# Kernel tuning notes

Hardware: AMD Instinct MI355X
Metric: run time of the kernel (lower is better)

## Reference

```python
import jax, jax.numpy as jnp
import numpy as np

N = 20000
E = 320000
IN_DIM, HID, OUT_DIM = 32, 64, 4
HEADS = 4
NEG_SLOPE = 0.2


def _self_loops(src, dst):
    loop = jnp.arange(N, dtype=src.dtype)
    return jnp.concatenate([src, loop]), jnp.concatenate([dst, loop])


def gcn_conv(x, W, b, src, dst):
    h = x @ W                                            # [N, C]
    es, ed = _self_loops(src, dst)
    deg = jax.ops.segment_sum(jnp.ones_like(es, dtype=h.dtype), ed, num_segments=N)
    dinv = jnp.where(deg > 0, jax.lax.rsqrt(deg), 0.0)
    norm = dinv[es] * dinv[ed]                           # [E']
    out = jax.ops.segment_sum(h[es] * norm[:, None], ed, num_segments=N)
    return out + b


def gat_conv(x, W, att_src, att_dst, b, src, dst):
    # PyG GATConv: heads concat, self-loops, leaky_relu(0.2), softmax over incoming edges per dst
    H, C = att_src.shape
    h = (x @ W).reshape(N, H, C)                         # [N, H, C]
    a_s = jnp.sum(h * att_src, axis=-1)                  # [N, H]
    a_d = jnp.sum(h * att_dst, axis=-1)                  # [N, H]
    es, ed = _self_loops(src, dst)
    logits = jax.nn.leaky_relu(a_s[es] + a_d[ed], NEG_SLOPE)   # [E', H]
    m = jax.ops.segment_max(logits, ed, num_segments=N)
    expv = jnp.exp(logits - m[ed])
    denom = jax.ops.segment_sum(expv, ed, num_segments=N)
    alpha = expv / denom[ed]                             # [E', H]
    out = jax.ops.segment_sum(h[es] * alpha[:, :, None], ed, num_segments=N)
    return out.reshape(N, H * C) + b


def setup_inputs() -> dict:
    key = jax.random.key(0)
    ks = iter(jax.random.split(key, 32))
    s = 0.05
    def w(shape):
        return jax.random.normal(next(ks), shape, dtype=jnp.float32) * s
    inp = {}
    inp["x"] = jax.random.normal(next(ks), (N, IN_DIM), dtype=jnp.float32)
    inp["edge_index"] = jax.random.randint(next(ks), (2, E), 0, N, dtype=jnp.int32)
    # encoder1 GCN 32->64; encoder2 GCN 64->128; encoder3 GAT 128->128 x4 heads
    inp["w_e1"], inp["b_e1"] = w((IN_DIM, HID)), jnp.zeros((HID,), jnp.float32)
    inp["w_e2"], inp["b_e2"] = w((HID, 2 * HID)), jnp.zeros((2 * HID,), jnp.float32)
    inp["w_e3"] = w((2 * HID, HEADS * 2 * HID))
    inp["as_e3"], inp["ad_e3"] = w((HEADS, 2 * HID)), w((HEADS, 2 * HID))
    inp["b_e3"] = jnp.zeros((HEADS * 2 * HID,), jnp.float32)
    # decoder1 GCN 1024->128; decoder2 GCN 128->64; decoder3 GAT 64->64 x4 heads
    inp["w_d1"], inp["b_d1"] = w((HEADS * 2 * HID, 2 * HID)), jnp.zeros((2 * HID,), jnp.float32)
    inp["w_d2"], inp["b_d2"] = w((2 * HID, HID)), jnp.zeros((HID,), jnp.float32)
    inp["w_d3"] = w((HID, HEADS * HID))
    inp["as_d3"], inp["ad_d3"] = w((HEADS, HID)), w((HEADS, HID))
    inp["b_d3"] = jnp.zeros((HEADS * HID,), jnp.float32)
    # MLP head 256->256->128->4
    inp["w_fc1"], inp["b_fc1"] = w((4 * HID, 4 * HID)), jnp.zeros((4 * HID,), jnp.float32)
    inp["w_fc2"], inp["b_fc2"] = w((4 * HID, 2 * HID)), jnp.zeros((2 * HID,), jnp.float32)
    inp["w_fin"], inp["b_fin"] = w((2 * HID, OUT_DIM)), jnp.zeros((OUT_DIM,), jnp.float32)
    return inp


def reference(x, edge_index, w_e1, b_e1, w_e2, b_e2, w_e3, as_e3, ad_e3, b_e3,
              w_d1, b_d1, w_d2, b_d2, w_d3, as_d3, ad_d3, b_d3,
              w_fc1, b_fc1, w_fc2, b_fc2, w_fin, b_fin):
    src, dst = edge_index[0], edge_index[1]
    relu = jax.nn.relu
    x1 = relu(gcn_conv(x, w_e1, b_e1, src, dst))
    x2 = relu(gcn_conv(x1, w_e2, b_e2, src, dst))
    x3 = relu(gat_conv(x2, w_e3, as_e3, ad_e3, b_e3, src, dst))
    h = relu(gcn_conv(x3, w_d1, b_d1, src, dst)) + x2
    h = relu(gcn_conv(h, w_d2, b_d2, src, dst)) + x1
    h = relu(gat_conv(h, w_d3, as_d3, ad_d3, b_d3, src, dst))
    h = relu(h @ w_fc1 + b_fc1)
    h = relu(h @ w_fc2 + b_fc2)
    return h @ w_fin + b_fin
```

## Files before the change

### kernel.cpp

```cpp
#include <hip/hip_runtime.h>
#include <cstdint>
#include <cstddef>

static constexpr int Nn = 20000;
static constexpr int Ee = 320000;

typedef _Float16 half8 __attribute__((ext_vector_type(8)));
typedef float f32x4 __attribute__((ext_vector_type(4)));

__device__ __forceinline__ float lrelu02(float x){ return fmaxf(x, 0.2f*x); }
__device__ __forceinline__ float af(int x){ return __int_as_float(x); }

__device__ __forceinline__ void packhl(float v, unsigned short& h, unsigned short& l){
  _Float16 hh = (_Float16)v;
  _Float16 ll = (_Float16)((v - (float)hh) * 2048.0f);
  h = __builtin_bit_cast(unsigned short, hh);
  l = __builtin_bit_cast(unsigned short, ll);
}

__global__ void k_count(const int* __restrict__ dst, int* __restrict__ cnt){
  int e = blockIdx.x*256 + threadIdx.x;
  if (e < Ee) atomicAdd(&cnt[dst[e]], 1);
}

__global__ void k_scan(const int* __restrict__ cnt, int* __restrict__ row_start,
                       float* __restrict__ dinv){
  __shared__ int part[1024];
  int tid = threadIdx.x;
  const int PER = 20;
  int base = tid*PER;
  int s = 0;
  for (int i = 0; i < PER; ++i){ int idx = base+i; if (idx < Nn) s += cnt[idx]; }
  part[tid] = s; __syncthreads();
  for (int off = 1; off < 1024; off <<= 1){
    int v = (tid >= off) ? part[tid-off] : 0;
    __syncthreads();
    part[tid] += v;
    __syncthreads();
  }
  int run = (tid == 0) ? 0 : part[tid-1];
  for (int i = 0; i < PER; ++i){
    int idx = base+i;
    if (idx < Nn){
      row_start[idx] = run;
      int c = cnt[idx];
      run += c;
      dinv[idx] = rsqrtf((float)(c+1));
    }
  }
  if (tid == 1023) row_start[Nn] = run;
}

__global__ void k_scatter(const int* __restrict__ src, const int* __restrict__ dst,
                          const int* __restrict__ row_start, int* __restrict__ fill,
                          int* __restrict__ csr){
  int e = blockIdx.x*256 + threadIdx.x;
  if (e < Ee){
    int d = dst[e];
    int pos = row_start[d] + atomicAdd(&fill[d], 1);
    csr[pos] = src[e];
  }
}

__global__ void k_erec(const int* __restrict__ csr, const float* __restrict__ dinv,
                       int2* __restrict__ erec){
  int i = blockIdx.x*256 + threadIdx.x;
  if (i < Ee){
    int u = csr[i];
    erec[i] = make_int2(u, __float_as_int(dinv[u]));
  }
}

template<int K, int J>
__global__ void k_packwf(const float* __restrict__ W, unsigned short* __restrict__ out){
  int i = blockIdx.x*256 + threadIdx.x;
  if (i < K*J){
    int k = i / J, col = i - k*J;
    unsigned short h, l; packhl(W[i], h, l);
    size_t pos = ((size_t)((col>>4)*(K/8) + (k>>3))*16 + (col&15))*8 + (k&7);
    out[pos] = h;
    out[pos + (size_t)K*J] = l;
  }
}

template<int C, int POST>
__global__ __launch_bounds__(256) void k_gcn_agg(
    const float* __restrict__ h, const float* __restrict__ dinv,
    const int* __restrict__ row_start, const int2* __restrict__ erec,
    const float* __restrict__ bias, const float* __restrict__ skip,
    float* __restrict__ outf, unsigned short* __restrict__ outp){
  int v = blockIdx.x*4 + (threadIdx.x >> 6);
  int lane = threadIdx.x & 63;
  int s = __builtin_amdgcn_readfirstlane(row_start[v]);
  int e = __builtin_amdgcn_readfirstlane(row_start[v+1]);
  float dv = dinv[v];
  const int c = (C==32) ? (lane & 31) : ((C==128) ? lane*2 : lane);

  float a0 = 0.f, a1 = 0.f;
  if constexpr (C == 32){
    int half = lane >> 5;
    int j = s + half;
    for (; j + 2 < e; j += 4){
      int2 r0 = erec[j], r1 = erec[j+2];
      float t0 = h[(size_t)r0.x*32 + c];
      float t1 = h[(size_t)r1.x*32 + c];
      a0 = fmaf(af(r0.y), t0, a0);
      a0 = fmaf(af(r1.y), t1, a0);
    }
    if (j < e){
      int2 r0 = erec[j];
      a0 = fmaf(af(r0.y), h[(size_t)r0.x*32 + c], a0);
    }
    a0 += __shfl_xor(a0, 32);
  } else if constexpr (C == 128){
    int j = s;
    for (; j + 4 <= e; j += 4){
      int2 r0 = erec[j], r1 = erec[j+1], r2 = erec[j+2], r3 = erec[j+3];
      float2 t0 = *(const float2*)&h[(size_t)r0.x*128 + c];
      float2 t1 = *(const float2*)&h[(size_t)r1.x*128 + c];
      float2 t2 = *(const float2*)&h[(size_t)r2.x*128 + c];
      float2 t3 = *(const float2*)&h[(size_t)r3.x*128 + c];
      a0=fmaf(af(r0.y),t0.x,a0); a1=fmaf(af(r0.y),t0.y,a1);
      a0=fmaf(af(r1.y),t1.x,a0); a1=fmaf(af(r1.y),t1.y,a1);
      a0=fmaf(af(r2.y),t2.x,a0); a1=fmaf(af(r2.y),t2.y,a1);
      a0=fmaf(af(r3.y),t3.x,a0); a1=fmaf(af(r3.y),t3.y,a1);
    }
    for (; j < e; ++j){
      int2 r = erec[j];
      float2 t = *(const float2*)&h[(size_t)r.x*128 + c];
      a0 = fmaf(af(r.y), t.x, a0); a1 = fmaf(af(r.y), t.y, a1);
    }
  } else {
    int j = s;
    for (; j + 4 <= e; j += 4){
      int2 r0 = erec[j], r1 = erec[j+1], r2 = erec[j+2], r3 = erec[j+3];
      float t0 = h[(size_t)r0.x*64 + c];
      float t1 = h[(size_t)r1.x*64 + c];
      float t2 = h[(size_t)r2.x*64 + c];
      float t3 = h[(size_t)r3.x*64 + c];
      a0=fmaf(af(r0.y),t0,a0); a0=fmaf(af(r1.y),t1,a0);
      a0=fmaf(af(r2.y),t2,a0); a0=fmaf(af(r3.y),t3,a0);
    }
    for (; j < e; ++j){
      int2 r = erec[j];
      a0 = fmaf(af(r.y), h[(size_t)r.x*64 + c], a0);
    }
  }

  if constexpr (C == 128){
    float2 hv = *(const float2*)&h[(size_t)v*128 + c];
    float vx = fmaf(a0, dv, hv.x*dv*dv);
    float vy = fmaf(a1, dv, hv.y*dv*dv);
    if constexpr (POST & 1){
      float2 bv = *(const float2*)&bias[c];
      float2 sk = *(const float2*)&skip[(size_t)v*128 + c];
      vx = fmaxf(vx + bv.x, 0.f) + sk.x;
      vy = fmaxf(vy + bv.y, 0.f) + sk.y;
    }
    if constexpr (POST & 2){
      unsigned short h0,l0,h1,l1; packhl(vx,h0,l0); packhl(vy,h1,l1);
      *(unsigned int*)&outp[(size_t)v*128 + c] = (unsigned)h0 | ((unsigned)h1<<16);
      *(unsigned int*)&outp[(size_t)v*128 + c + (size_t)Nn*128] = (unsigned)l0 | ((unsigned)l1<<16);
    } else {
      *(float2*)&outf[(size_t)v*128 + c] = make_float2(vx, vy);
    }
  } else if constexpr (C == 64){
    float val = fmaf(a0, dv, h[(size_t)v*64 + c]*dv*dv);
    if constexpr (POST & 1){
      val = fmaxf(val + bias[c], 0.f) + skip[(size_t)v*64 + c];
    }
    if constexpr (POST & 2){
      unsigned short hh,ll; packhl(val,hh,ll);
      outp[(size_t)v*64 + c] = hh;
      outp[(size_t)v*64 + c + (size_t)Nn*64] = ll;
    } else {
      outf[(size_t)v*64 + c] = val;
    }
  } else {
    float val = fmaf(a0, dv, h[(size_t)v*32 + c]*dv*dv);
    if (lane < 32){
      unsigned short hh,ll; packhl(val,hh,ll);
      outp[(size_t)v*32 + c] = hh;
      outp[(size_t)v*32 + c + (size_t)Nn*32] = ll;
    }
  }
}

template<int INC, int C>
__global__ void k_fold(const float* __restrict__ W, const float* __restrict__ as_,
                       const float* __restrict__ ad_, float* __restrict__ wsF,
                       float* __restrict__ wdF){
  int h = threadIdx.x >> 6, lane = threadIdx.x & 63;
  for (int k = lane; k < INC; k += 64){
    float s = 0.f, d = 0.f;
    #pragma unroll 4
    for (int c = 0; c < C; ++c){
      float wv = W[(size_t)k*(4*C) + h*C + c];
      s = fmaf(wv, as_[h*C + c], s);
      d = fmaf(wv, ad_[h*C + c], d);
    }
    wsF[h*INC + k] = s;
    wdF[h*INC + k] = d;
  }
}

template<int INC>
__global__ __launch_bounds__(256) void k_attn_in(
    const float* __restrict__ X, const float* __restrict__ wsF, const float* __restrict__ wdF,
    float* __restrict__ aS, float* __restrict__ aD){
  int v = blockIdx.x*4 + (threadIdx.x >> 6);
  int lane = threadIdx.x & 63;
  float x0 = X[(size_t)v*INC + lane];
  float x1 = (INC == 128) ? X[(size_t)v*INC + 64 + lane] : 0.f;
  float s[4], d[4];
  #pragma unroll
  for (int h = 0; h < 4; ++h){
    s[h] = x0*wsF[h*INC + lane];
    d[h] = x0*wdF[h*INC + lane];
    if constexpr (INC == 128){
      s[h] = fmaf(x1, wsF[h*INC + 64 + lane], s[h]);
      d[h] = fmaf(x1, wdF[h*INC + 64 + lane], d[h]);
    }
  }
  #pragma unroll
  for (int off = 32; off; off >>= 1){
    #pragma unroll
    for (int h = 0; h < 4; ++h){
      s[h] += __shfl_xor(s[h], off);
      d[h] += __shfl_xor(d[h], off);
    }
  }
  if (lane == 0){
    *(float4*)&aS[v*4] = make_float4(s[0], s[1], s[2], s[3]);
    *(float4*)&aD[v*4] = make_float4(d[0], d[1], d[2], d[3]);
  }
}

__global__ __launch_bounds__(256) void k_gat_prep(
    const float* __restrict__ aS, const float* __restrict__ aD,
    const int* __restrict__ row_start, const int* __restrict__ csr,
    float4* __restrict__ alphaE, float4* __restrict__ fS4, float4* __restrict__ rin4){
  int v = blockIdx.x*4 + (threadIdx.x >> 6);
  int lane = threadIdx.x & 63;
  int s = row_start[v], e = row_start[v+1];

  float4 tD = *(const float4*)&aD[v*4];
  float ad0=tD.x, ad1=tD.y, ad2=tD.z, ad3=tD.w;
  float4 tS = *(const float4*)&aS[v*4];
  float ls0=lrelu02(tS.x+ad0), ls1=lrelu02(tS.y+ad1), ls2=lrelu02(tS.z+ad2), ls3=lrelu02(tS.w+ad3);

  float m0=ls0, m1=ls1, m2=ls2, m3=ls3;
  for (int i = s + lane; i < e; i += 64){
    int u = csr[i];
    float4 a4 = *(const float4*)&aS[u*4];
    m0 = fmaxf(m0, lrelu02(a4.x+ad0));
    m1 = fmaxf(m1, lrelu02(a4.y+ad1));
    m2 = fmaxf(m2, lrelu02(a4.z+ad2));
    m3 = fmaxf(m3, lrelu02(a4.w+ad3));
  }
  #pragma unroll
  for (int off = 32; off; off >>= 1){
    m0 = fmaxf(m0, __shfl_xor(m0, off));
    m1 = fmaxf(m1, __shfl_xor(m1, off));
    m2 = fmaxf(m2, __shfl_xor(m2, off));
    m3 = fmaxf(m3, __shfl_xor(m3, off));
  }

  float sd0=0.f, sd1=0.f, sd2=0.f, sd3=0.f;
  for (int i = s + lane; i < e; i += 64){
    int u = csr[i];
    float4 a4 = *(const float4*)&aS[u*4];
    float f0 = __expf(lrelu02(a4.x+ad0) - m0);
    float f1 = __expf(lrelu02(a4.y+ad1) - m1);
    float f2 = __expf(lrelu02(a4.z+ad2) - m2);
    float f3 = __expf(lrelu02(a4.w+ad3) - m3);
    sd0 += f0; sd1 += f1; sd2 += f2; sd3 += f3;
    alphaE[i] = make_float4(f0, f1, f2, f3);
  }
  #pragma unroll
  for (int off = 32; off; off >>= 1){
    sd0 += __shfl_xor(sd0, off);
    sd1 += __shfl_xor(sd1, off);
    sd2 += __shfl_xor(sd2, off);
    sd3 += __shfl_xor(sd3, off);
  }
  if (lane == 0){
    float es0=__expf(ls0-m0), es1=__expf(ls1-m1), es2=__expf(ls2-m2), es3=__expf(ls3-m3);
    fS4[v] = make_float4(es0, es1, es2, es3);
    rin4[v] = make_float4(1.f/(sd0+es0), 1.f/(sd1+es1), 1.f/(sd2+es2), 1.f/(sd3+es3));
  }
}

template<int INC>
__global__ __launch_bounds__(256) void k_gat_agg2(
    const float* __restrict__ X, const int* __restrict__ csr,
    const float4* __restrict__ alphaE, const float4* __restrict__ fS4,
    const float4* __restrict__ rin4, const int* __restrict__ row_start,
    unsigned short* __restrict__ outp){
  int v = blockIdx.x*4 + (threadIdx.x >> 6);
  int lane = threadIdx.x & 63;
  int s = __builtin_amdgcn_readfirstlane(row_start[v]);
  int e = __builtin_amdgcn_readfirstlane(row_start[v+1]);
  const int c2 = lane*2;

  float2 acc0={0,0}, acc1={0,0}, acc2={0,0}, acc3={0,0};
  float ac0=0.f, ac1=0.f, ac2=0.f, ac3=0.f;

  int j = s;
  for (; j + 4 <= e; j += 4){
    int u0=csr[j], u1=csr[j+1], u2=csr[j+2], u3=csr[j+3];
    float4 f0=alphaE[j], f1=alphaE[j+1], f2=alphaE[j+2], f3=alphaE[j+3];
    if constexpr (INC == 128){
      float2 x0 = *(const float2*)&X[(size_t)u0*128 + c2];
      float2 x1 = *(const float2*)&X[(size_t)u1*128 + c2];
      float2 x2 = *(const float2*)&X[(size_t)u2*128 + c2];
      float2 x3 = *(const float2*)&X[(size_t)u3*128 + c2];
      acc0.x=fmaf(f0.x,x0.x,acc0.x); acc0.y=fmaf(f0.x,x0.y,acc0.y);
      acc1.x=fmaf(f0.y,x0.x,acc1.x); acc1.y=fmaf(f0.y,x0.y,acc1.y);
      acc2.x=fmaf(f0.z,x0.x,acc2.x); acc2.y=fmaf(f0.z,x0.y,acc2.y);
      acc3.x=fmaf(f0.w,x0.x,acc3.x); acc3.y=fmaf(f0.w,x0.y,acc3.y);
      acc0.x=fmaf(f1.x,x1.x,acc0.x); acc0.y=fmaf(f1.x,x1.y,acc0.y);
      acc1.x=fmaf(f1.y,x1.x,acc1.x); acc1.y=fmaf(f1.y,x1.y,acc1.y);
      acc2.x=fmaf(f1.z,x1.x,acc2.x); acc2.y=fmaf(f1.z,x1.y,acc2.y);
      acc3.x=fmaf(f1.w,x1.x,acc3.x); acc3.y=fmaf(f1.w,x1.y,acc3.y);
      acc0.x=fmaf(f2.x,x2.x,acc0.x); acc0.y=fmaf(f2.x,x2.y,acc0.y);
      acc1.x=fmaf(f2.y,x2.x,acc1.x); acc1.y=fmaf(f2.y,x2.y,acc1.y);
      acc2.x=fmaf(f2.z,x2.x,acc2.x); acc2.y=fmaf(f2.z,x2.y,acc2.y);
      acc3.x=fmaf(f2.w,x2.x,acc3.x); acc3.y=fmaf(f2.w,x2.y,acc3.y);
      acc0.x=fmaf(f3.x,x3.x,acc0.x); acc0.y=fmaf(f3.x,x3.y,acc0.y);
      acc1.x=fmaf(f3.y,x3.x,acc1.x); acc1.y=fmaf(f3.y,x3.y,acc1.y);
      acc2.x=fmaf(f3.z,x3.x,acc2.x); acc2.y=fmaf(f3.z,x3.y,acc2.y);
      acc3.x=fmaf(f3.w,x3.x,acc3.x); acc3.y=fmaf(f3.w,x3.y,acc3.y);
    } else {
      float x0 = X[(size_t)u0*64 + lane];
      float x1 = X[(size_t)u1*64 + lane];
      float x2 = X[(size_t)u2*64 + lane];
      float x3 = X[(size_t)u3*64 + lane];
      ac0=fmaf(f0.x,x0,ac0); ac1=fmaf(f0.y,x0,ac1); ac2=fmaf(f0.z,x0,ac2); ac3=fmaf(f0.w,x0,ac3);
      ac0=fmaf(f1.x,x1,ac0); ac1=fmaf(f1.y,x1,ac1); ac2=fmaf(f1.z,x1,ac2); ac3=fmaf(f1.w,x1,ac3);
      ac0=fmaf(f2.x,x2,ac0); ac1=fmaf(f2.y,x2,ac1); ac2=fmaf(f2.z,x2,ac2); ac3=fmaf(f2.w,x2,ac3);
      ac0=fmaf(f3.x,x3,ac0); ac1=fmaf(f3.y,x3,ac1); ac2=fmaf(f3.z,x3,ac2); ac3=fmaf(f3.w,x3,ac3);
    }
  }
  for (; j < e; ++j){
    int u = csr[j];
    float4 f = alphaE[j];
    if constexpr (INC == 128){
      float2 xu = *(const float2*)&X[(size_t)u*128 + c2];
      acc0.x=fmaf(f.x,xu.x,acc0.x); acc0.y=fmaf(f.x,xu.y,acc0.y);
      acc1.x=fmaf(f.y,xu.x,acc1.x); acc1.y=fmaf(f.y,xu.y,acc1.y);
      acc2.x=fmaf(f.z,xu.x,acc2.x); acc2.y=fmaf(f.z,xu.y,acc2.y);
      acc3.x=fmaf(f.w,xu.x,acc3.x); acc3.y=fmaf(f.w,xu.y,acc3.y);
    } else {
      float xu = X[(size_t)u*64 + lane];
      ac0=fmaf(f.x,xu,ac0); ac1=fmaf(f.y,xu,ac1); ac2=fmaf(f.z,xu,ac2); ac3=fmaf(f.w,xu,ac3);
    }
  }

  float4 fs = fS4[v];
  float4 rv = rin4[v];

  if constexpr (INC == 128){
    float2 xv = *(const float2*)&X[(size_t)v*128 + c2];
    const size_t loOff = (size_t)Nn*512;
    float ox, oy; unsigned short h0,l0,h1,l1;
    ox=(acc0.x+fs.x*xv.x)*rv.x; oy=(acc0.y+fs.x*xv.y)*rv.x;
    packhl(ox,h0,l0); packhl(oy,h1,l1);
    *(unsigned int*)&outp[(size_t)v*512 +   0 + c2] = (unsigned)h0|((unsigned)h1<<16);
    *(unsigned int*)&outp[(size_t)v*512 +   0 + c2 + loOff] = (unsigned)l0|((unsigned)l1<<16);
    ox=(acc1.x+fs.y*xv.x)*rv.y; oy=(acc1.y+fs.y*xv.y)*rv.y;
    packhl(ox,h0,l0); packhl(oy,h1,l1);
    *(unsigned int*)&outp[(size_t)v*512 + 128 + c2] = (unsigned)h0|((unsigned)h1<<16);
    *(unsigned int*)&outp[(size_t)v*512 + 128 + c2 + loOff] = (unsigned)l0|((unsigned)l1<<16);
    ox=(acc2.x+fs.z*xv.x)*rv.z; oy=(acc2.y+fs.z*xv.y)*rv.z;
    packhl(ox,h0,l0); packhl(oy,h1,l1);
    *(unsigned int*)&outp[(size_t)v*512 + 256 + c2] = (unsigned)h0|((unsigned)h1<<16);
    *(unsigned int*)&outp[(size_t)v*512 + 256 + c2 + loOff] = (unsigned)l0|((unsigned)l1<<16);
    ox=(acc3.x+fs.w*xv.x)*rv.w; oy=(acc3.y+fs.w*xv.y)*rv.w;
    packhl(ox,h0,l0); packhl(oy,h1,l1);
    *(unsigned int*)&outp[(size_t)v*512 + 384 + c2] = (unsigned)h0|((unsigned)h1<<16);
    *(unsigned int*)&outp[(size_t)v*512 + 384 + c2 + loOff] = (unsigned)l0|((unsigned)l1<<16);
  } else {
    float xv = X[(size_t)v*64 + lane];
    const size_t loOff = (size_t)Nn*256;
    unsigned short hh,ll;
    float o;
    o = (ac0+fs.x*xv)*rv.x; packhl(o,hh,ll);
    outp[(size_t)v*256 +   0 + lane] = hh; outp[(size_t)v*256 +   0 + lane + loOff] = ll;
    o = (ac1+fs.y*xv)*rv.y; packhl(o,hh,ll);
    outp[(size_t)v*256 +  64 + lane] = hh; outp[(size_t)v*256 +  64 + lane + loOff] = ll;
    o = (ac2+fs.z*xv)*rv.z; packhl(o,hh,ll);
    outp[(size_t)v*256 + 128 + lane] = hh; outp[(size_t)v*256 + 128 + lane + loOff] = ll;
    o = (ac3+fs.w*xv)*rv.w; packhl(o,hh,ll);
    outp[(size_t)v*256 + 192 + lane] = hh; outp[(size_t)v*256 + 192 + lane + loOff] = ll;
  }
}

template<int K, int J, int Jh, int EPI>
__global__ __launch_bounds__(256) void k_gemm(
    const unsigned short* __restrict__ Ahi, int lda,
    const unsigned short* __restrict__ Wp,
    const float* __restrict__ bias,
    float* __restrict__ outf, unsigned short* __restrict__ outp){
  __shared__ unsigned short sAhi[2*64*8], sAlo[2*64*8];
  __shared__ unsigned short sBhi[4*64*8], sBlo[4*64*8];

  const int tid  = threadIdx.x;
  const int lane = tid & 63, w = tid >> 6;
  const int rh = w & 1, ch = w >> 1;
  const int rb = blockIdx.x;
  const int colbase = blockIdx.z*Jh + blockIdx.y*64;
  const int akoff   = blockIdx.z*K;
  const size_t AloOff = (size_t)Nn*lda;
  const size_t WloOff = (size_t)K*J;

  f32x4 accH0 = {0,0,0,0}, accH1 = {0,0,0,0};
  f32x4 accM0 = {0,0,0,0}, accM1 = {0,0,0,0};

  const int arow = tid >> 3;
  const int ak4  = (tid & 7) * 4;
  const int aw_idx = (((arow>>4)*4 + (ak4>>3))*16 + (arow&15))*8 + (ak4&4);
  const unsigned short* Ag = Ahi + (size_t)(rb*32 + arow)*lda + akoff + ak4;
  const int bcol = tid & 63;
  const int bkg  = tid >> 6;
  const int bw_idx = (((bcol>>4)*4 + bkg)*16 + (bcol&15))*8;
  const int cf_g  = (colbase>>4) + (bcol>>4);
  const size_t wbase = ((size_t)cf_g*(K/8)*16 + (size_t)(bcol&15))*8;

  #pragma unroll 1
  for (int ks = 0; ks < K/32; ++ks){
    if (ks) __syncthreads();
    {
      const unsigned short* p = Ag + ks*32;
      uint2 hv = *(const uint2*)p;
      uint2 lv = *(const uint2*)(p + AloOff);
      *(uint2*)&sAhi[aw_idx] = hv;
      *(uint2*)&sAlo[aw_idx] = lv;
    }
    {
      size_t goff = wbase + (size_t)(ks*4 + bkg)*16*8;
      uint4 hv = *(const uint4*)&Wp[goff];
      uint4 lv = *(const uint4*)&Wp[goff + WloOff];
      *(uint4*)&sBhi[bw_idx] = hv;
      *(uint4*)&sBlo[bw_idx] = lv;
    }
    __syncthreads();

    half8 aH = *(const half8*)&sAhi[(rh*64 + lane)*8];
    half8 aL = *(const half8*)&sAlo[(rh*64 + lane)*8];
    {
      int cf = ch*2;
      half8 bH = *(const half8*)&sBhi[(cf*64 + lane)*8];
      half8 bL = *(const half8*)&sBlo[(cf*64 + lane)*8];
      accH0 = __builtin_amdgcn_mfma_f32_16x16x32_f16(aH, bH, accH0, 0, 0, 0);
      accM0 = __builtin_amdgcn_mfma_f32_16x16x32_f16(aH, bL, accM0, 0, 0, 0);
      accM0 = __builtin_amdgcn_mfma_f32_16x16x32_f16(aL, bH, accM0, 0, 0, 0);
    }
    {
      int cf = ch*2 + 1;
      half8 bH = *(const half8*)&sBhi[(cf*64 + lane)*8];
      half8 bL = *(const half8*)&sBlo[(cf*64 + lane)*8];
      accH1 = __builtin_amdgcn_mfma_f32_16x16x32_f16(aH, bH, accH1, 0, 0, 0);
      accM1 = __builtin_amdgcn_mfma_f32_16x16x32_f16(aH, bL, accM1, 0, 0, 0);
      accM1 = __builtin_amdgcn_mfma_f32_16x16x32_f16(aL, bH, accM1, 0, 0, 0);
    }
  }

  #pragma unroll
  for (int q = 0; q < 2; ++q){
    int cf = ch*2 + q;
    int col = colbase + cf*16 + (lane & 15);
    float bv = (EPI >= 1) ? bias[col] : 0.f;
    const f32x4& aH = q ? accH1 : accH0;
    const f32x4& aM = q ? accM1 : accM0;
    #pragma unroll
    for (int r = 0; r < 4; ++r){
      int row = rb*32 + rh*16 + ((lane>>4)*4 + r);
      float v = aH[r] + aM[r]*(1.0f/2048.0f);
      if constexpr (EPI >= 1) v = fmaxf(v + bv, 0.f);
      if constexpr (EPI == 2){
        unsigned short hh, ll; packhl(v, hh, ll);
        outp[(size_t)row*J + col] = hh;
        outp[(size_t)row*J + col + (size_t)Nn*J] = ll;
      } else {
        outf[(size_t)row*J + col] = v;
      }
    }
  }
}

__global__ __launch_bounds__(256) void k_mm_fin(
    const float* __restrict__ A, const float* __restrict__ W,
    const float* __restrict__ bias, float* __restrict__ out){
  int row = blockIdx.x*4 + (threadIdx.x >> 6);
  int lane = threadIdx.x & 63;
  float a0 = A[(size_t)row*128 + lane];
  float a1 = A[(size_t)row*128 + 64 + lane];
  float4 w0 = ((const float4*)W)[lane];
  float4 w1 = ((const float4*)W)[64 + lane];
  float p0 = fmaf(a1, w1.x, a0*w0.x);
  float p1 = fmaf(a1, w1.y, a0*w0.y);
  float p2 = fmaf(a1, w1.z, a0*w0.z);
  float p3 = fmaf(a1, w1.w, a0*w0.w);
  #pragma unroll
  for (int off = 32; off; off >>= 1){
    p0 += __shfl_xor(p0, off);
    p1 += __shfl_xor(p1, off);
    p2 += __shfl_xor(p2, off);
    p3 += __shfl_xor(p3, off);
  }
  if (lane == 0){
    float4 bv = *(const float4*)bias;
    *(float4*)&out[(size_t)row*4] = make_float4(p0+bv.x, p1+bv.y, p2+bv.z, p3+bv.w);
  }
}

extern "C" void kernel_launch(void* const* d_in, const int* in_sizes, int n_in,
                              void* d_out, int out_size, void* d_ws, size_t ws_size,
                              hipStream_t stream){
  const float* x     = (const float*)d_in[0];
  const int*   ei    = (const int*)  d_in[1];
  const float* w_e1  = (const float*)d_in[2];
  const float* b_e1  = (const float*)d_in[3];
  const float* w_e2  = (const float*)d_in[4];
  const float* b_e2  = (const float*)d_in[5];
  const float* w_e3  = (const float*)d_in[6];
  const float* as_e3 = (const float*)d_in[7];
  const float* ad_e3 = (const float*)d_in[8];
  const float* b_e3  = (const float*)d_in[9];
  const float* w_d1  = (const float*)d_in[10];
  const float* b_d1  = (const float*)d_in[11];
  const float* w_d2  = (const float*)d_in[12];
  const float* b_d2  = (const float*)d_in[13];
  const float* w_d3  = (const float*)d_in[14];
  const float* as_d3 = (const float*)d_in[15];
  const float* ad_d3 = (const float*)d_in[16];
  const float* b_d3  = (const float*)d_in[17];
  const float* w_fc1 = (const float*)d_in[18];
  const float* b_fc1 = (const float*)d_in[19];
  const float* w_fc2 = (const float*)d_in[20];
  const float* b_fc2 = (const float*)d_in[21];
  const float* w_fin = (const float*)d_in[22];
  const float* b_fin = (const float*)d_in[23];

  char* ws = (char*)d_ws;
  size_t off = 0;
  auto alloc = [&](size_t bytes)->char*{
    char* p = ws + off;
    off += (bytes + 127) & ~size_t(127);
    return p;
  };
  int*   cnt       = (int*)  alloc((size_t)Nn*4);
  int*   fill      = (int*)  alloc((size_t)Nn*4);
  int*   row_start = (int*)  alloc((size_t)(Nn+1)*4);
  int*   csr       = (int*)  alloc((size_t)Ee*4);
  float* dinv      = (float*)alloc((size_t)Nn*4);
  int2*  erec      = (int2*) alloc((size_t)Ee*8);
  float4* alphaE   = (float4*)alloc((size_t)Ee*16);
  float4* fS4      = (float4*)alloc((size_t)Nn*16);
  float4* rin4     = (float4*)alloc((size_t)Nn*16);
  float* aSb       = (float*)alloc((size_t)Nn*16);
  float* aDb       = (float*)alloc((size_t)Nn*16);
  float* wsF_e3    = (float*)alloc(4*128*4);
  float* wdF_e3    = (float*)alloc(4*128*4);
  float* wsF_d3    = (float*)alloc(4*64*4);
  float* wdF_d3    = (float*)alloc(4*64*4);
  unsigned short* wp_e1  = (unsigned short*)alloc((size_t)32*64*4);
  unsigned short* wp_e2  = (unsigned short*)alloc((size_t)64*128*4);
  unsigned short* wp_e3  = (unsigned short*)alloc((size_t)128*512*4);
  unsigned short* wp_d1  = (unsigned short*)alloc((size_t)512*128*4);
  unsigned short* wp_d2  = (unsigned short*)alloc((size_t)128*64*4);
  unsigned short* wp_d3  = (unsigned short*)alloc((size_t)64*256*4);
  unsigned short* wp_fc1 = (unsigned short*)alloc((size_t)256*256*4);
  unsigned short* wp_fc2 = (unsigned short*)alloc((size_t)256*128*4);
  unsigned short* P0 = (unsigned short*)alloc((size_t)Nn*32*4);
  float* X1 = (float*)alloc((size_t)Nn*64*4);
  float* X2 = (float*)alloc((size_t)Nn*128*4);
  unsigned short* S1 = (unsigned short*)alloc((size_t)Nn*512*4);
  unsigned short* S2 = (unsigned short*)alloc((size_t)Nn*512*4);
  char*  S3 = alloc((size_t)Nn*128*4);

  const int* srcp = ei;
  const int* dstp = ei + Ee;

  hipMemsetAsync(cnt, 0, (size_t)Nn*4, stream);
  hipMemsetAsync(fill, 0, (size_t)Nn*4, stream);
  k_count<<<(Ee+255)/256, 256, 0, stream>>>(dstp, cnt);
  k_scan<<<1, 1024, 0, stream>>>(cnt, row_start, dinv);
  k_scatter<<<(Ee+255)/256, 256, 0, stream>>>(srcp, dstp, row_start, fill, csr);
  k_erec<<<(Ee+255)/256, 256, 0, stream>>>(csr, dinv, erec);
  k_fold<128,128><<<1, 256, 0, stream>>>(w_e3, as_e3, ad_e3, wsF_e3, wdF_e3);
  k_fold<64,64><<<1, 256, 0, stream>>>(w_d3, as_d3, ad_d3, wsF_d3, wdF_d3);
  k_packwf<32,64>  <<<  8, 256, 0, stream>>>(w_e1,  wp_e1);
  k_packwf<64,128> <<< 32, 256, 0, stream>>>(w_e2,  wp_e2);
  k_packwf<128,512><<<256, 256, 0, stream>>>(w_e3,  wp_e3);
  k_packwf<512,128><<<256, 256, 0, stream>>>(w_d1,  wp_d1);
  k_packwf<128,64> <<< 32, 256, 0, stream>>>(w_d2,  wp_d2);
  k_packwf<64,256> <<< 64, 256, 0, stream>>>(w_d3,  wp_d3);
  k_packwf<256,256><<<256, 256, 0, stream>>>(w_fc1, wp_fc1);
  k_packwf<256,128><<<128, 256, 0, stream>>>(w_fc2, wp_fc2);

  k_gcn_agg<32,2><<<Nn/4, 256, 0, stream>>>(x, dinv, row_start, erec, nullptr, nullptr, nullptr, P0);
  k_gemm<32,64,64,1><<<dim3(625,1,1), 256, 0, stream>>>(P0, 32, wp_e1, b_e1, X1, nullptr);
  k_gcn_agg<64,2><<<Nn/4, 256, 0, stream>>>(X1, dinv, row_start, erec, nullptr, nullptr, nullptr, (unsigned short*)S3);
  k_gemm<64,128,128,1><<<dim3(625,2,1), 256, 0, stream>>>((unsigned short*)S3, 64, wp_e2, b_e2, X2, nullptr);
  k_attn_in<128><<<Nn/4, 256, 0, stream>>>(X2, wsF_e3, wdF_e3, aSb, aDb);
  k_gat_prep<<<Nn/4, 256, 0, stream>>>(aSb, aDb, row_start, csr, alphaE, fS4, rin4);
  k_gat_agg2<128><<<Nn/4, 256, 0, stream>>>(X2, csr, alphaE, fS4, rin4, row_start, S1);
  k_gemm<128,512,128,2><<<dim3(625,2,4), 256, 0, stream>>>(S1, 512, wp_e3, b_e3, nullptr, S2);
  k_gemm<512,128,128,0><<<dim3(625,2,1), 256, 0, stream>>>(S2, 512, wp_d1, nullptr, (float*)S3, nullptr);
  k_gcn_agg<128,3><<<Nn/4, 256, 0, stream>>>((float*)S3, dinv, row_start, erec, b_d1, X2, nullptr, S1);
  k_gemm<128,64,64,0><<<dim3(625,1,1), 256, 0, stream>>>(S1, 128, wp_d2, nullptr, (float*)S2, nullptr);
  k_gcn_agg<64,1><<<Nn/4, 256, 0, stream>>>((float*)S2, dinv, row_start, erec, b_d2, X1, (float*)S3, nullptr);
  k_attn_in<64><<<Nn/4, 256, 0, stream>>>((float*)S3, wsF_d3, wdF_d3, aSb, aDb);
  k_gat_prep<<<Nn/4, 256, 0, stream>>>(aSb, aDb, row_start, csr, alphaE, fS4, rin4);
  k_gat_agg2<64><<<Nn/4, 256, 0, stream>>>((float*)S3, csr, alphaE, fS4, rin4, row_start, S1);
  k_gemm<64,256,64,2><<<dim3(625,1,4), 256, 0, stream>>>(S1, 256, wp_d3, b_d3, nullptr, S2);
  k_gemm<256,256,256,2><<<dim3(625,4,1), 256, 0, stream>>>(S2, 256, wp_fc1, b_fc1, nullptr, S1);
  k_gemm<256,128,128,1><<<dim3(625,2,1), 256, 0, stream>>>(S1, 256, wp_fc2, b_fc2, (float*)S2, nullptr);
  k_mm_fin<<<Nn/4, 256, 0, stream>>>((float*)S2, w_fin, b_fin, (float*)d_out);
}
```

Baseline: 396.2 us.

## Store activations in MFMA fragment layout and drop LDS staging in GEMM

Producers of packed fp16 hi/lo activations now write them directly in a 16x8 MFMA-fragment tiled layout, with the row count padded to a multiple of 16. The GEMM kernel then loads A and B fragments straight from global memory into registers, with no shared-memory staging or barriers. Each wave now computes four 16-column tiles, with a configurable rows-per-wave split, and launch grids are reshaped to match. The erec-building kernel is also folded into the scatter kernel to save a launch and a pass over csr. The cost is more redundant global/L2 fragment loads across waves in place of LDS reuse.

```diff
diff --git a/kernel.cpp b/kernel.cpp
--- a/kernel.cpp
+++ b/kernel.cpp
@@ -4,6 +4,7 @@
 
 static constexpr int Nn = 20000;
 static constexpr int Ee = 320000;
+static constexpr int Npad = 20032;
 
 typedef _Float16 half8 __attribute__((ext_vector_type(8)));
 typedef float f32x4 __attribute__((ext_vector_type(4)));
@@ -16,6 +17,10 @@
   _Float16 ll = (_Float16)((v - (float)hh) * 2048.0f);
   h = __builtin_bit_cast(unsigned short, hh);
   l = __builtin_bit_cast(unsigned short, ll);
+}
+
+__device__ __forceinline__ size_t fragaddr(int row, int k, int lda){
+  return ((size_t)(row>>4)*(lda>>3) + (k>>3))*128 + (size_t)(row&15)*8 + (k&7);
 }
 
 __global__ void k_count(const int* __restrict__ dst, int* __restrict__ cnt){
@@ -53,21 +58,15 @@
 
 __global__ void k_scatter(const int* __restrict__ src, const int* __restrict__ dst,
                           const int* __restrict__ row_start, int* __restrict__ fill,
-                          int* __restrict__ csr){
+                          int* __restrict__ csr, const float* __restrict__ dinv,
+                          int2* __restrict__ erec){
   int e = blockIdx.x*256 + threadIdx.x;
   if (e < Ee){
     int d = dst[e];
     int pos = row_start[d] + atomicAdd(&fill[d], 1);
-    csr[pos] = src[e];
-  }
-}
-
-__global__ void k_erec(const int* __restrict__ csr, const float* __restrict__ dinv,
-                       int2* __restrict__ erec){
-  int i = blockIdx.x*256 + threadIdx.x;
-  if (i < Ee){
-    int u = csr[i];
-    erec[i] = make_int2(u, __float_as_int(dinv[u]));
+    int u = src[e];
+    csr[pos] = u;
+    erec[pos] = make_int2(u, __float_as_int(dinv[u]));
   }
 }
 
@@ -159,8 +158,9 @@
     }
     if constexpr (POST & 2){
       unsigned short h0,l0,h1,l1; packhl(vx,h0,l0); packhl(vy,h1,l1);
-      *(unsigned int*)&outp[(size_t)v*128 + c] = (unsigned)h0 | ((unsigned)h1<<16);
-      *(unsigned int*)&outp[(size_t)v*128 + c + (size_t)Nn*128] = (unsigned)l0 | ((unsigned)l1<<16);
+      size_t a = fragaddr(v, c, 128);
+      *(unsigned int*)&outp[a] = (unsigned)h0 | ((unsigned)h1<<16);
+      *(unsigned int*)&outp[a + (size_t)Npad*128] = (unsigned)l0 | ((unsigned)l1<<16);
     } else {
       *(float2*)&outf[(size_t)v*128 + c] = make_float2(vx, vy);
     }
@@ -171,8 +171,9 @@
     }
     if constexpr (POST & 2){
       unsigned short hh,ll; packhl(val,hh,ll);
-      outp[(size_t)v*64 + c] = hh;
-      outp[(size_t)v*64 + c + (size_t)Nn*64] = ll;
+      size_t a = fragaddr(v, c, 64);
+      outp[a] = hh;
+      outp[a + (size_t)Npad*64] = ll;
     } else {
       outf[(size_t)v*64 + c] = val;
     }
@@ -180,8 +181,9 @@
     float val = fmaf(a0, dv, h[(size_t)v*32 + c]*dv*dv);
     if (lane < 32){
       unsigned short hh,ll; packhl(val,hh,ll);
-      outp[(size_t)v*32 + c] = hh;
-      outp[(size_t)v*32 + c + (size_t)Nn*32] = ll;
+      size_t a = fragaddr(v, c, 32);
+      outp[a] = hh;
+      outp[a + (size_t)Npad*32] = ll;
     }
   }
 }
@@ -362,128 +364,94 @@
 
   if constexpr (INC == 128){
     float2 xv = *(const float2*)&X[(size_t)v*128 + c2];
-    const size_t loOff = (size_t)Nn*512;
+    const size_t loOff = (size_t)Npad*512;
     float ox, oy; unsigned short h0,l0,h1,l1;
-    ox=(acc0.x+fs.x*xv.x)*rv.x; oy=(acc0.y+fs.x*xv.y)*rv.x;
-    packhl(ox,h0,l0); packhl(oy,h1,l1);
-    *(unsigned int*)&outp[(size_t)v*512 +   0 + c2] = (unsigned)h0|((unsigned)h1<<16);
-    *(unsigned int*)&outp[(size_t)v*512 +   0 + c2 + loOff] = (unsigned)l0|((unsigned)l1<<16);
-    ox=(acc1.x+fs.y*xv.x)*rv.y; oy=(acc1.y+fs.y*xv.y)*rv.y;
-    packhl(ox,h0,l0); packhl(oy,h1,l1);
-    *(unsigned int*)&outp[(size_t)v*512 + 128 + c2] = (unsigned)h0|((unsigned)h1<<16);
-    *(unsigned int*)&outp[(size_t)v*512 + 128 + c2 + loOff] = (unsigned)l0|((unsigned)l1<<16);
-    ox=(acc2.x+fs.z*xv.x)*rv.z; oy=(acc2.y+fs.z*xv.y)*rv.z;
-    packhl(ox,h0,l0); packhl(oy,h1,l1);
-    *(unsigned int*)&outp[(size_t)v*512 + 256 + c2] = (unsigned)h0|((unsigned)h1<<16);
-    *(unsigned int*)&outp[(size_t)v*512 + 256 + c2 + loOff] = (unsigned)l0|((unsigned)l1<<16);
-    ox=(acc3.x+fs.w*xv.x)*rv.w; oy=(acc3.y+fs.w*xv.y)*rv.w;
-    packhl(ox,h0,l0); packhl(oy,h1,l1);
-    *(unsigned int*)&outp[(size_t)v*512 + 384 + c2] = (unsigned)h0|((unsigned)h1<<16);
-    *(unsigned int*)&outp[(size_t)v*512 + 384 + c2 + loOff] = (unsigned)l0|((unsigned)l1<<16);
+    float fsx[4] = {fs.x, fs.y, fs.z, fs.w};
+    float rvx[4] = {rv.x, rv.y, rv.z, rv.w};
+    float2 accs[4] = {acc0, acc1, acc2, acc3};
+    #pragma unroll
+    for (int hh = 0; hh < 4; ++hh){
+      ox=(accs[hh].x+fsx[hh]*xv.x)*rvx[hh]; oy=(accs[hh].y+fsx[hh]*xv.y)*rvx[hh];
+      packhl(ox,h0,l0); packhl(oy,h1,l1);
+      size_t a = fragaddr(v, hh*128 + c2, 512);
+      *(unsigned int*)&outp[a] = (unsigned)h0|((unsigned)h1<<16);
+      *(unsigned int*)&outp[a + loOff] = (unsigned)l0|((unsigned)l1<<16);
+    }
   } else {
     float xv = X[(size_t)v*64 + lane];
-    const size_t loOff = (size_t)Nn*256;
-    unsigned short hh,ll;
-    float o;
-    o = (ac0+fs.x*xv)*rv.x; packhl(o,hh,ll);
-    outp[(size_t)v*256 +   0 + lane] = hh; outp[(size_t)v*256 +   0 + lane + loOff] = ll;
-    o = (ac1+fs.y*xv)*rv.y; packhl(o,hh,ll);
-    outp[(size_t)v*256 +  64 + lane] = hh; outp[(size_t)v*256 +  64 + lane + loOff] = ll;
-    o = (ac2+fs.z*xv)*rv.z; packhl(o,hh,ll);
-    outp[(size_t)v*256 + 128 + lane] = hh; outp[(size_t)v*256 + 128 + lane + loOff] = ll;
-    o = (ac3+fs.w*xv)*rv.w; packhl(o,hh,ll);
-    outp[(size_t)v*256 + 192 + lane] = hh; outp[(size_t)v*256 + 192 + lane + loOff] = ll;
-  }
-}
-
-template<int K, int J, int Jh, int EPI>
+    const size_t loOff = (size_t)Npad*256;
+    float fsx[4] = {fs.x, fs.y, fs.z, fs.w};
+    float rvx[4] = {rv.x, rv.y, rv.z, rv.w};
+    float acx[4] = {ac0, ac1, ac2, ac3};
+    #pragma unroll
+    for (int hh = 0; hh < 4; ++hh){
+      unsigned short hhh, lll;
+      float o = (acx[hh]+fsx[hh]*xv)*rvx[hh];
+      packhl(o,hhh,lll);
+      size_t a = fragaddr(v, hh*64 + lane, 256);
+      outp[a] = hhh; outp[a + loOff] = lll;
+    }
+  }
+}
+
+template<int K, int J, int Jh, int RW, int EPI>
 __global__ __launch_bounds__(256) void k_gemm(
-    const unsigned short* __restrict__ Ahi, int lda,
+    const unsigned short* __restrict__ Ap, int lda,
     const unsigned short* __restrict__ Wp,
     const float* __restrict__ bias,
     float* __restrict__ outf, unsigned short* __restrict__ outp){
-  __shared__ unsigned short sAhi[2*64*8], sAlo[2*64*8];
-  __shared__ unsigned short sBhi[4*64*8], sBlo[4*64*8];
-
   const int tid  = threadIdx.x;
   const int lane = tid & 63, w = tid >> 6;
-  const int rh = w & 1, ch = w >> 1;
-  const int rb = blockIdx.x;
-  const int colbase = blockIdx.z*Jh + blockIdx.y*64;
+  const int wr = w % RW, wc = w / RW;
+  const int rowbase = blockIdx.x*(16*RW) + wr*16;
+  const int colbase = blockIdx.z*Jh + blockIdx.y*(64*(4/RW)) + wc*64;
   const int akoff   = blockIdx.z*K;
-  const size_t AloOff = (size_t)Nn*lda;
+  const size_t AloOff = (size_t)Npad*lda;
   const size_t WloOff = (size_t)K*J;
-
-  f32x4 accH0 = {0,0,0,0}, accH1 = {0,0,0,0};
-  f32x4 accM0 = {0,0,0,0}, accM1 = {0,0,0,0};
-
-  const int arow = tid >> 3;
-  const int ak4  = (tid & 7) * 4;
-  const int aw_idx = (((arow>>4)*4 + (ak4>>3))*16 + (arow&15))*8 + (ak4&4);
-  const unsigned short* Ag = Ahi + (size_t)(rb*32 + arow)*lda + akoff + ak4;
-  const int bcol = tid & 63;
-  const int bkg  = tid >> 6;
-  const int bw_idx = (((bcol>>4)*4 + bkg)*16 + (bcol&15))*8;
-  const int cf_g  = (colbase>>4) + (bcol>>4);
-  const size_t wbase = ((size_t)cf_g*(K/8)*16 + (size_t)(bcol&15))*8;
-
-  #pragma unroll 1
+  const int l15 = lane & 15, lg = lane >> 4;
+
+  const unsigned short* Abase =
+      Ap + ((size_t)(rowbase>>4)*(lda>>3) + (akoff>>3) + lg)*128 + (size_t)l15*8;
+  const int cfg0 = colbase >> 4;
+
+  f32x4 accH[4] = {{0,0,0,0},{0,0,0,0},{0,0,0,0},{0,0,0,0}};
+  f32x4 accM[4] = {{0,0,0,0},{0,0,0,0},{0,0,0,0},{0,0,0,0}};
+
+  #pragma unroll 2
   for (int ks = 0; ks < K/32; ++ks){
-    if (ks) __syncthreads();
-    {
-      const unsigned short* p = Ag + ks*32;
-      uint2 hv = *(const uint2*)p;
-      uint2 lv = *(const uint2*)(p + AloOff);
-      *(uint2*)&sAhi[aw_idx] = hv;
-      *(uint2*)&sAlo[aw_idx] = lv;
-    }
-    {
-      size_t goff = wbase + (size_t)(ks*4 + bkg)*16*8;
-      uint4 hv = *(const uint4*)&Wp[goff];
-      uint4 lv = *(const uint4*)&Wp[goff + WloOff];
-      *(uint4*)&sBhi[bw_idx] = hv;
-      *(uint4*)&sBlo[bw_idx] = lv;
-    }
-    __syncthreads();
-
-    half8 aH = *(const half8*)&sAhi[(rh*64 + lane)*8];
-    half8 aL = *(const half8*)&sAlo[(rh*64 + lane)*8];
-    {
-      int cf = ch*2;
-      half8 bH = *(const half8*)&sBhi[(cf*64 + lane)*8];
-      half8 bL = *(const half8*)&sBlo[(cf*64 + lane)*8];
-      accH0 = __builtin_amdgcn_mfma_f32_16x16x32_f16(aH, bH, accH0, 0, 0, 0);
-      accM0 = __builtin_amdgcn_mfma_f32_16x16x32_f16(aH, bL, accM0, 0, 0, 0);
-      accM0 = __builtin_amdgcn_mfma_f32_16x16x32_f16(aL, bH, accM0, 0, 0, 0);
-    }
-    {
-      int cf = ch*2 + 1;
-      half8 bH = *(const half8*)&sBhi[(cf*64 + lane)*8];
-      half8 bL = *(const half8*)&sBlo[(cf*64 + lane)*8];
-      accH1 = __builtin_amdgcn_mfma_f32_16x16x32_f16(aH, bH, accH1, 0, 0, 0);
-      accM1 = __builtin_amdgcn_mfma_f32_16x16x32_f16(aH, bL, accM1, 0, 0, 0);
-      accM1 = __builtin_amdgcn_mfma_f32_16x16x32_f16(aL, bH, accM1, 0, 0, 0);
+    const unsigned short* ap = Abase + (size_t)ks*4*128;
+    half8 aH = __builtin_bit_cast(half8, *(const uint4*)ap);
+    half8 aL = __builtin_bit_cast(half8, *(const uint4*)(ap + AloOff));
+    #pragma unroll
+    for (int cf = 0; cf < 4; ++cf){
+      const unsigned short* bp =
+          Wp + ((size_t)(cfg0+cf)*(K/8) + ks*4 + lg)*128 + (size_t)l15*8;
+      half8 bH = __builtin_bit_cast(half8, *(const uint4*)bp);
+      half8 bL = __builtin_bit_cast(half8, *(const uint4*)(bp + WloOff));
+      accH[cf] = __builtin_amdgcn_mfma_f32_16x16x32_f16(aH, bH, accH[cf], 0, 0, 0);
+      accM[cf] = __builtin_amdgcn_mfma_f32_16x16x32_f16(aH, bL, accM[cf], 0, 0, 0);
+      accM[cf] = __builtin_amdgcn_mfma_f32_16x16x32_f16(aL, bH, accM[cf], 0, 0, 0);
     }
   }
 
   #pragma unroll
-  for (int q = 0; q < 2; ++q){
-    int cf = ch*2 + q;
-    int col = colbase + cf*16 + (lane & 15);
+  for (int cf = 0; cf < 4; ++cf){
+    int col = colbase + cf*16 + l15;
     float bv = (EPI >= 1) ? bias[col] : 0.f;
-    const f32x4& aH = q ? accH1 : accH0;
-    const f32x4& aM = q ? accM1 : accM0;
     #pragma unroll
     for (int r = 0; r < 4; ++r){
-      int row = rb*32 + rh*16 + ((lane>>4)*4 + r);
-      float v = aH[r] + aM[r]*(1.0f/2048.0f);
-      if constexpr (EPI >= 1) v = fmaxf(v + bv, 0.f);
-      if constexpr (EPI == 2){
-        unsigned short hh, ll; packhl(v, hh, ll);
-        outp[(size_t)row*J + col] = hh;
-        outp[(size_t)row*J + col + (size_t)Nn*J] = ll;
-      } else {
-        outf[(size_t)row*J + col] = v;
+      int row = rowbase + lg*4 + r;
+      if (row < Nn){
+        float v = accH[cf][r] + accM[cf][r]*(1.0f/2048.0f);
+        if constexpr (EPI >= 1) v = fmaxf(v + bv, 0.f);
+        if constexpr (EPI == 2){
+          unsigned short hh, ll; packhl(v, hh, ll);
+          size_t a = fragaddr(row, col, J);
+          outp[a] = hh;
+          outp[a + (size_t)Npad*J] = ll;
+        } else {
+          outf[(size_t)row*J + col] = v;
+        }
       }
     }
   }
@@ -547,7 +515,7 @@
   size_t off = 0;
   auto alloc = [&](size_t bytes)->char*{
     char* p = ws + off;
-    off += (bytes + 127) & ~size_t(127);
+    off += (bytes + 255) & ~size_t(255);
     return p;
   };
   int*   cnt       = (int*)  alloc((size_t)Nn*4);
@@ -573,12 +541,12 @@
   unsigned short* wp_d3  = (unsigned short*)alloc((size_t)64*256*4);
   unsigned short* wp_fc1 = (unsigned short*)alloc((size_t)256*256*4);
   unsigned short* wp_fc2 = (unsigned short*)alloc((size_t)256*128*4);
-  unsigned short* P0 = (unsigned short*)alloc((size_t)Nn*32*4);
+  unsigned short* P0 = (unsigned short*)alloc((size_t)Npad*32*4);
   float* X1 = (float*)alloc((size_t)Nn*64*4);
   float* X2 = (float*)alloc((size_t)Nn*128*4);
-  unsigned short* S1 = (unsigned short*)alloc((size_t)Nn*512*4);
-  unsigned short* S2 = (unsigned short*)alloc((size_t)Nn*512*4);
-  char*  S3 = alloc((size_t)Nn*128*4);
+  unsigned short* S1 = (unsigned short*)alloc((size_t)Npad*512*4);
+  unsigned short* S2 = (unsigned short*)alloc((size_t)Npad*512*4);
+  char*  S3 = alloc((size_t)Npad*128*4);
 
   const int* srcp = ei;
   const int* dstp = ei + Ee;
@@ -587,8 +555,7 @@
   hipMemsetAsync(fill, 0, (size_t)Nn*4, stream);
   k_count<<<(Ee+255)/256, 256, 0, stream>>>(dstp, cnt);
   k_scan<<<1, 1024, 0, stream>>>(cnt, row_start, dinv);
-  k_scatter<<<(Ee+255)/256, 256, 0, stream>>>(srcp, dstp, row_start, fill, csr);
-  k_erec<<<(Ee+255)/256, 256, 0, stream>>>(csr, dinv, erec);
+  k_scatter<<<(Ee+255)/256, 256, 0, stream>>>(srcp, dstp, row_start, fill, csr, dinv, erec);
   k_fold<128,128><<<1, 256, 0, stream>>>(w_e3, as_e3, ad_e3, wsF_e3, wdF_e3);
   k_fold<64,64><<<1, 256, 0, stream>>>(w_d3, as_d3, ad_d3, wsF_d3, wdF_d3);
   k_packwf<32,64>  <<<  8, 256, 0, stream>>>(w_e1,  wp_e1);
@@ -601,22 +568,22 @@
   k_packwf<256,128><<<128, 256, 0, stream>>>(w_fc2, wp_fc2);
 
   k_gcn_agg<32,2><<<Nn/4, 256, 0, stream>>>(x, dinv, row_start, erec, nullptr, nullptr, nullptr, P0);
-  k_gemm<32,64,64,1><<<dim3(625,1,1), 256, 0, stream>>>(P0, 32, wp_e1, b_e1, X1, nullptr);
+  k_gemm<32,64,64,4,1><<<dim3(313,1,1), 256, 0, stream>>>(P0, 32, wp_e1, b_e1, X1, nullptr);
   k_gcn_agg<64,2><<<Nn/4, 256, 0, stream>>>(X1, dinv, row_start, erec, nullptr, nullptr, nullptr, (unsigned short*)S3);
-  k_gemm<64,128,128,1><<<dim3(625,2,1), 256, 0, stream>>>((unsigned short*)S3, 64, wp_e2, b_e2, X2, nullptr);
+  k_gemm<64,128,128,2,1><<<dim3(626,1,1), 256, 0, stream>>>((unsigned short*)S3, 64, wp_e2, b_e2, X2, nullptr);
   k_attn_in<128><<<Nn/4, 256, 0, stream>>>(X2, wsF_e3, wdF_e3, aSb, aDb);
   k_gat_prep<<<Nn/4, 256, 0, stream>>>(aSb, aDb, row_start, csr, alphaE, fS4, rin4);
   k_gat_agg2<128><<<Nn/4, 256, 0, stream>>>(X2, csr, alphaE, fS4, rin4, row_start, S1);
-  k_gemm<128,512,128,2><<<dim3(625,2,4), 256, 0, stream>>>(S1, 512, wp_e3, b_e3, nullptr, S2);
-  k_gemm<512,128,128,0><<<dim3(625,2,1), 256, 0, stream>>>(S2, 512, wp_d1, nullptr, (float*)S3, nullptr);
+  k_gemm<128,512,128,2,2><<<dim3(626,1,4), 256, 0, stream>>>(S1, 512, wp_e3, b_e3, nullptr, S2);
+  k_gemm<512,128,128,2,0><<<dim3(626,1,1), 256, 0, stream>>>(S2, 512, wp_d1, nullptr, (float*)S3, nullptr);
   k_gcn_agg<128,3><<<Nn/4, 256, 0, stream>>>((float*)S3, dinv, row_start, erec, b_d1, X2, nullptr, S1);
-  k_gemm<128,64,64,0><<<dim3(625,1,1), 256, 0, stream>>>(S1, 128, wp_d2, nullptr, (float*)S2, nullptr);
+  k_gemm<128,64,64,4,0><<<dim3(313,1,1), 256, 0, stream>>>(S1, 128, wp_d2, nullptr, (float*)S2, nullptr);
   k_gcn_agg<64,1><<<Nn/4, 256, 0, stream>>>((float*)S2, dinv, row_start, erec, b_d2, X1, (float*)S3, nullptr);
   k_attn_in<64><<<Nn/4, 256, 0, stream>>>((float*)S3, wsF_d3, wdF_d3, aSb, aDb);
   k_gat_prep<<<Nn/4, 256, 0, stream>>>(aSb, aDb, row_start, csr, alphaE, fS4, rin4);
   k_gat_agg2<64><<<Nn/4, 256, 0, stream>>>((float*)S3, csr, alphaE, fS4, rin4, row_start, S1);
-  k_gemm<64,256,64,2><<<dim3(625,1,4), 256, 0, stream>>>(S1, 256, wp_d3, b_d3, nullptr, S2);
-  k_gemm<256,256,256,2><<<dim3(625,4,1), 256, 0, stream>>>(S2, 256, wp_fc1, b_fc1, nullptr, S1);
-  k_gemm<256,128,128,1><<<dim3(625,2,1), 256, 0, stream>>>(S1, 256, wp_fc2, b_fc2, (float*)S2, nullptr);
+  k_gemm<64,256,64,4,2><<<dim3(313,1,4), 256, 0, stream>>>(S1, 256, wp_d3, b_d3, nullptr, S2);
+  k_gemm<256,256,256,2,2><<<dim3(626,2,1), 256, 0, stream>>>(S2, 256, wp_fc1, b_fc1, nullptr, S1);
+  k_gemm<256,128,128,2,1><<<dim3(626,1,1), 256, 0, stream>>>(S1, 256, wp_fc2, b_fc2, (float*)S2, nullptr);
   k_mm_fin<<<Nn/4, 256, 0, stream>>>((float*)S2, w_fin, b_fin, (float*)d_out);
 }
```

Result: slower. 434.2 us (+9.6%).
